# Kernel tuning notes

Hardware: AMD Instinct MI355X
Metric: run time of the kernel (lower is better)

The kernel has to match this reference:

```python
import jax, jax.numpy as jnp
import numpy as np

D_MODEL = 1024
NUM_HEADS = 16
D_K = D_MODEL // NUM_HEADS
S, B = 2048, 2


def setup_inputs() -> dict:
    key = jax.random.key(0)
    ks = jax.random.split(key, 11)
    lim = 1.0 / np.sqrt(D_MODEL)
    def lin(kw, kb):
        W = jax.random.uniform(kw, (D_MODEL, D_MODEL), jnp.float32, -lim, lim)
        b = jax.random.uniform(kb, (D_MODEL,), jnp.float32, -lim, lim)
        return W, b
    Wq, bq = lin(ks[0], ks[1])
    Wk, bk = lin(ks[2], ks[3])
    Wv, bv = lin(ks[4], ks[5])
    Wo, bo = lin(ks[6], ks[7])
    q = jax.random.normal(ks[8], (S, B, D_MODEL), jnp.float32)
    k = jax.random.normal(ks[9], (S, B, D_MODEL), jnp.float32)
    v = jax.random.normal(ks[10], (S, B, D_MODEL), jnp.float32)
    return {"q": q, "k": k, "v": v,
            "Wq": Wq, "bq": bq, "Wk": Wk, "bk": bk,
            "Wv": Wv, "bv": bv, "Wo": Wo, "bo": bo}


def reference(q, k, v, Wq, bq, Wk, bk, Wv, bv, Wo, bo):
    s, b, _ = q.shape
    scale = np.sqrt(D_K).astype(np.float32)
    # torch Linear: x @ W.T + b
    def proj(x, W, bias):
        y = jnp.einsum('sbd,ed->sbe', x, W) + bias
        # [S,B,D] -> [B,H,S,d_k]
        return y.reshape(s, b, NUM_HEADS, D_K).transpose(1, 2, 0, 3)
    Q = proj(q, Wq, bq)
    K = proj(k, Wk, bk)
    V = proj(v, Wv, bv)
    scores = jnp.einsum('bhsd,bhtd->bhst', Q, K) / scale  # [B,H,S,S]
    attn = jax.nn.softmax(scores, axis=-1)
    ctx = jnp.einsum('bhst,bhtd->bhsd', attn, V)  # [B,H,S,d_k]
    ctx = ctx.transpose(2, 0, 1, 3).reshape(s, b, NUM_HEADS * D_K)
    return jnp.einsum('sbd,ed->sbe', ctx, Wo) + bo
```

## Files before the change

kernel.cpp:

```cpp
#include <hip/hip_runtime.h>
#include <stdint.h>

typedef __attribute__((ext_vector_type(8))) short short8;
typedef __attribute__((ext_vector_type(4))) float f32x4;
typedef __attribute__((ext_vector_type(16))) float f32x16;

#define MFMA16(a, b, c) __builtin_amdgcn_mfma_f32_16x16x32_bf16((a), (b), (c), 0, 0, 0)
#define MFMA32(a, b, c) __builtin_amdgcn_mfma_f32_32x32x16_bf16((a), (b), (c), 0, 0, 0)

__device__ inline unsigned short f2bf(float x) {
  unsigned u = __float_as_uint(x);
  u = (u + 0x7FFFu + ((u >> 16) & 1u)) >> 16;
  return (unsigned short)u;
}

__device__ inline void gload16(const unsigned short* g, unsigned short* l) {
  __builtin_amdgcn_global_load_lds(
      (const __attribute__((address_space(1))) unsigned int*)g,
      (__attribute__((address_space(3))) unsigned int*)l, 16, 0, 0);
}

__device__ inline short8 lds8(const unsigned short* base, int byteoff) {
  return *reinterpret_cast<const short8*>(reinterpret_cast<const char*>(base) + byteoff);
}

__device__ inline unsigned cvtpk(float lo, float hi) {
  unsigned r;
  asm("v_cvt_pk_bf16_f32 %0, %1, %2" : "=v"(r) : "v"(lo), "v"(hi));
  return r;
}
__device__ inline void plswap(unsigned& a, unsigned& b) {
  asm volatile("v_permlane32_swap_b32 %0, %1" : "+v"(a), "+v"(b));
}
__device__ inline float swapadd(float v) {
  float a = v, b;
  asm volatile("v_mov_b32 %1, %0\n\tv_permlane32_swap_b32 %0, %1" : "+v"(a), "=&v"(b));
  return a + b;
}

__device__ inline short8 mk8(unsigned a, unsigned b, unsigned c, unsigned d) {
  union { unsigned u[4]; short8 v; } x;
  x.u[0] = a; x.u[1] = b; x.u[2] = c; x.u[3] = d;
  return x.v;
}

__device__ inline int swz(int row, int chunk) {
  return row * 128 + (((chunk) ^ (row & 7)) << 4);
}

__device__ inline void exppack(const f32x16& sv, float& lsum, short8& paLo, short8& paHi) {
  float p[16];
#pragma unroll
  for (int i = 0; i < 16; ++i) p[i] = __builtin_amdgcn_exp2f(sv[i]);
  float q8[8];
#pragma unroll
  for (int i = 0; i < 8; ++i) q8[i] = p[2 * i] + p[2 * i + 1];
#pragma unroll
  for (int s2 = 4; s2 > 0; s2 >>= 1)
#pragma unroll
    for (int i = 0; i < s2; ++i) q8[i] += q8[i + s2];
  lsum += q8[0];
  unsigned w0 = cvtpk(p[0], p[1]), w1 = cvtpk(p[2], p[3]);
  unsigned w2 = cvtpk(p[4], p[5]), w3 = cvtpk(p[6], p[7]);
  plswap(w0, w2); plswap(w1, w3);
  unsigned w4 = cvtpk(p[8], p[9]), w5 = cvtpk(p[10], p[11]);
  unsigned w6 = cvtpk(p[12], p[13]), w7 = cvtpk(p[14], p[15]);
  plswap(w4, w6); plswap(w5, w7);
  paLo = mk8(w0, w1, w2, w3);
  paHi = mk8(w4, w5, w6, w7);
}

__global__ __launch_bounds__(256) void cvt_bf16x(const float* __restrict__ a0,
                                                 const float* __restrict__ a1,
                                                 const float* __restrict__ a2,
                                                 const float* __restrict__ a3,
                                                 unsigned short* __restrict__ d, int per) {
  int y = blockIdx.y;
  const float* s = (y == 0) ? a0 : (y == 1) ? a1 : (y == 2) ? a2 : a3;
  int i = (blockIdx.x * 256 + threadIdx.x) * 8;
  if (i >= per) return;
  float4 v0 = *reinterpret_cast<const float4*>(s + i);
  float4 v1 = *reinterpret_cast<const float4*>(s + i + 4);
  short8 o;
  o[0] = (short)f2bf(v0.x); o[1] = (short)f2bf(v0.y);
  o[2] = (short)f2bf(v0.z); o[3] = (short)f2bf(v0.w);
  o[4] = (short)f2bf(v1.x); o[5] = (short)f2bf(v1.y);
  o[6] = (short)f2bf(v1.z); o[7] = (short)f2bf(v1.w);
  *reinterpret_cast<short8*>(d + (size_t)y * per + i) = o;
}

template <int MODE>
__global__ __launch_bounds__(256) void gemm_bt(
    const unsigned short* __restrict__ Abase, const unsigned short* __restrict__ Wbase,
    const float* __restrict__ bias0, const float* __restrict__ bias1,
    const float* __restrict__ bias2, unsigned short* __restrict__ ObaseBf,
    float* __restrict__ ObaseF, int M, int N, int K) {
  constexpr int CHUNK = (MODE == 0) ? 192 : 64;

  const int orig = blockIdx.x;
  const int wg = (orig & 7) * CHUNK + (orig >> 3);
  int z, bx, by;
  if (MODE == 0) {
    z = wg >> 9;
    int r = wg & 511;
    by = r & 15;
    bx = r >> 4;
  } else {
    z = 0; by = wg & 15; bx = wg >> 4;
  }

  const unsigned short* A = Abase + (size_t)z * M * K;
  const unsigned short* W = Wbase + (size_t)z * N * K;
  const float* bias = (z == 0) ? bias0 : (z == 1 ? bias1 : bias2);

  __shared__ unsigned short As[2 * 128 * 64];
  __shared__ unsigned short Bs[2 * 64 * 64];

  const int t = threadIdx.x;
  const int lane = t & 63, w = t >> 6;
  const int wm = w >> 1, wn = w & 1;
  const int m0 = bx * 128, n0 = by * 64;
  const int lrow = lane & 15, lg = lane >> 4;

  f32x4 acc[4][2] = {};

  int arow[4], acol[4], brow[2], bcol[2];
#pragma unroll
  for (int p = 0; p < 4; ++p) {
    int c = (p * 4 + w) * 64 + lane;
    arow[p] = c >> 3; acol[p] = ((c & 7) ^ (arow[p] & 7)) * 8;
  }
#pragma unroll
  for (int p = 0; p < 2; ++p) {
    int c = (p * 4 + w) * 64 + lane;
    brow[p] = c >> 3; bcol[p] = ((c & 7) ^ (brow[p] & 7)) * 8;
  }

#define STAGE_G(kt, buf)                                                              \
  {                                                                                   \
    _Pragma("unroll") for (int p = 0; p < 4; ++p)                                     \
        gload16(&A[(size_t)(m0 + arow[p]) * K + (kt) + acol[p]],                      \
                &As[(buf)*8192 + ((p * 4 + w) * 64) * 8]);                            \
    _Pragma("unroll") for (int p = 0; p < 2; ++p)                                     \
        gload16(&W[(size_t)(n0 + brow[p]) * K + (kt) + bcol[p]],                      \
                &Bs[(buf)*4096 + ((p * 4 + w) * 64) * 8]);                            \
  }

#define COMPUTE(buf)                                                                  \
  {                                                                                   \
    _Pragma("unroll") for (int kc = 0; kc < 2; ++kc) {                                \
      short8 af[4], bfr[2];                                                           \
      _Pragma("unroll") for (int i = 0; i < 4; ++i)                                   \
          af[i] = lds8(As, (buf)*16384 + swz(wm * 64 + i * 16 + lrow, kc * 4 + lg));  \
      _Pragma("unroll") for (int i = 0; i < 2; ++i)                                   \
          bfr[i] = lds8(Bs, (buf)*8192 + swz(wn * 32 + i * 16 + lrow, kc * 4 + lg));  \
      _Pragma("unroll") for (int mi = 0; mi < 4; ++mi)                                \
          _Pragma("unroll") for (int ni = 0; ni < 2; ++ni)                            \
              acc[mi][ni] = MFMA16(af[mi], bfr[ni], acc[mi][ni]);                     \
    }                                                                                 \
  }

  STAGE_G(0, 0);
  asm volatile("s_waitcnt vmcnt(0)" ::: "memory");
  __builtin_amdgcn_s_barrier();
  __builtin_amdgcn_sched_barrier(0);

  int cur = 0;
  for (int kt = 0; kt < K - 64; kt += 64) {
    STAGE_G(kt + 64, cur ^ 1);
    COMPUTE(cur);
    asm volatile("s_waitcnt vmcnt(0)" ::: "memory");
    __builtin_amdgcn_s_barrier();
    __builtin_amdgcn_sched_barrier(0);
    cur ^= 1;
  }
  COMPUTE(cur);
#undef STAGE_G
#undef COMPUTE

  const int r0 = lg * 4;
  if (MODE == 0) {
    const float scale = (z == 0) ? 0.18033688011112042f : 1.0f;
    if (z < 2) {
      unsigned short* O = ObaseBf + (size_t)z * (size_t)M * N;
#pragma unroll
      for (int mi = 0; mi < 4; ++mi)
#pragma unroll
        for (int ni = 0; ni < 2; ++ni) {
          int e = n0 + wn * 32 + ni * 16 + lrow;
          float be = bias[e];
          int h = e >> 6, d = e & 63;
#pragma unroll
          for (int r = 0; r < 4; ++r) {
            int m = m0 + wm * 64 + mi * 16 + r0 + r;
            int s = m >> 1, bb = m & 1;
            O[(((size_t)(bb * 16 + h) * 2048 + s) << 6) + d] = f2bf((acc[mi][ni][r] + be) * scale);
          }
        }
    } else {
      __builtin_amdgcn_s_barrier();
      unsigned short* T = As;
      const int h = n0 >> 6;
#pragma unroll
      for (int mi = 0; mi < 4; ++mi)
#pragma unroll
        for (int ni = 0; ni < 2; ++ni) {
          int d = wn * 32 + ni * 16 + lrow;
          float be = bias[n0 + d];
#pragma unroll
          for (int r = 0; r < 4; ++r) {
            int mrel = wm * 64 + mi * 16 + r0 + r;
            int sl = mrel >> 1, bb = mrel & 1;
            T[(bb * 64 + d) * 72 + sl] = f2bf(acc[mi][ni][r] + be);
          }
        }
      __builtin_amdgcn_s_barrier();
      unsigned short* O = ObaseBf + (size_t)2 * (size_t)M * N;
#pragma unroll
      for (int pass = 0; pass < 4; ++pass) {
        int rr = pass * 32 + (t >> 3);
        int sl8 = (t & 7) * 8;
        short8 vv = *reinterpret_cast<const short8*>(&T[rr * 72 + sl8]);
        int bb = rr >> 6, d = rr & 63;
        *reinterpret_cast<short8*>(
            &O[(((size_t)(bb * 16 + h) * 64 + d) << 11) + (m0 >> 1) + sl8]) = vv;
      }
    }
  } else {
    float* O = ObaseF;
#pragma unroll
    for (int mi = 0; mi < 4; ++mi)
#pragma unroll
      for (int ni = 0; ni < 2; ++ni) {
        int e = n0 + wn * 32 + ni * 16 + lrow;
        float be = bias[e];
#pragma unroll
        for (int r = 0; r < 4; ++r) {
          int m = m0 + wm * 64 + mi * 16 + r0 + r;
          O[(size_t)m * N + e] = acc[mi][ni][r] + be;
        }
      }
  }
}

__global__ __launch_bounds__(256, 2) void attn(const unsigned short* __restrict__ Q,
                                               const unsigned short* __restrict__ K,
                                               const unsigned short* __restrict__ Vt,
                                               unsigned short* __restrict__ ctx) {
  __shared__ unsigned short Ks[2 * 8192];
  __shared__ unsigned short Vs[2 * 8192];

  const int orig = blockIdx.x;
  const int wg = ((orig & 7) << 6) + (orig >> 3);
  const int bh = wg >> 4;
  const int qb = wg & 15;

  const int t = threadIdx.x, lane = t & 63, wv = t >> 6;
  const int q0 = qb * 128 + wv * 32;
  const int q = lane & 31, hi = lane >> 5;
  const int fq = (q ^ (q >> 3)) & 7;

  const unsigned short* Qb = Q + ((size_t)bh * 2048 + q0) * 64;
  const unsigned short* Kb = K + (size_t)bh * 2048 * 64;
  const unsigned short* Vb = Vt + (size_t)bh * 64 * 2048;

  short8 qf[4];
#pragma unroll
  for (int m = 0; m < 4; ++m)
    qf[m] = *reinterpret_cast<const short8*>(&Qb[q * 64 + m * 16 + hi * 8]);

  int koff[4][4];
#pragma unroll
  for (int st = 0; st < 4; ++st) {
    int f = fq ^ ((st & 1) * 4);
#pragma unroll
    for (int m = 0; m < 4; ++m)
      koff[st][m] = (st * 32 + q) * 128 + (((m * 2 + hi) ^ f) << 4);
  }
  int voff[2][4][2];
#pragma unroll
  for (int dh = 0; dh < 2; ++dh) {
    int g = fq ^ (dh * 4);
#pragma unroll
    for (int st = 0; st < 4; ++st)
#pragma unroll
      for (int kc = 0; kc < 2; ++kc) {
        int cir = st * 4 + kc * 2 + hi;
        int scir = (cir & 8) | ((cir & 7) ^ g);
        voff[dh][st][kc] = (dh * 32 + q) * 256 + (scir << 4);
      }
  }

  const unsigned short* ksp[4];
  const unsigned short* vpp[4];
#pragma unroll
  for (int p = 0; p < 4; ++p) {
    int c = (p * 4 + wv) * 64 + lane;
    int kr = c >> 3, kcc = c & 7;
    int gk = (kr ^ (kr >> 3)) & 7;
    ksp[p] = Kb + (size_t)kr * 64 + (kcc ^ gk) * 8;
    int vr = c >> 4, cir = c & 15;
    int gv = (vr ^ (vr >> 3)) & 7;
    int scir = (cir & 8) | ((cir & 7) ^ gv);
    vpp[p] = Vb + (size_t)vr * 2048 + scir * 8;
  }

#define STAGE(buf)                                                           \
  {                                                                          \
    _Pragma("unroll") for (int p = 0; p < 4; ++p)                            \
        gload16(ksp[p], &Ks[(buf)*8192 + ((p * 4 + wv) * 64) * 8]);          \
    _Pragma("unroll") for (int p = 0; p < 4; ++p)                            \
        gload16(vpp[p], &Vs[(buf)*8192 + ((p * 4 + wv) * 64) * 8]);          \
    _Pragma("unroll") for (int p = 0; p < 4; ++p) { ksp[p] += 8192; vpp[p] += 128; } \
  }

#define QK(st, sv)                                                           \
  {                                                                          \
    _Pragma("unroll") for (int m = 0; m < 4; ++m)                            \
        sv = MFMA32(lds8(Ks, cb + koff[st][m]), qf[m], sv);                  \
  }

#define PV(st, pl, ph)                                                       \
  {                                                                          \
    oa0 = MFMA32(pl, lds8(Vs, cb + voff[0][st][0]), oa0);                    \
    oa1 = MFMA32(pl, lds8(Vs, cb + voff[1][st][0]), oa1);                    \
    oa0 = MFMA32(ph, lds8(Vs, cb + voff[0][st][1]), oa0);                    \
    oa1 = MFMA32(ph, lds8(Vs, cb + voff[1][st][1]), oa1);                    \
  }

  f32x16 oa0 = {}, oa1 = {};
  float lsum = 0.f;

  STAGE(0);
  asm volatile("s_waitcnt vmcnt(0)" ::: "memory");
  __builtin_amdgcn_s_barrier();
  __builtin_amdgcn_sched_barrier(0);

  for (int tile = 0; tile < 16; ++tile) {
    const int cb = (tile & 1) * 16384;
    if (tile < 15) STAGE((tile & 1) ^ 1);

    __builtin_amdgcn_s_setprio(1);
    f32x16 s0 = {}, s1 = {}, s2 = {}, s3 = {};
    short8 pl, ph;
    QK(0, s0);
    QK(1, s1);
    exppack(s0, lsum, pl, ph);
    PV(0, pl, ph);
    QK(2, s2);
    exppack(s1, lsum, pl, ph);
    PV(1, pl, ph);
    QK(3, s3);
    exppack(s2, lsum, pl, ph);
    PV(2, pl, ph);
    exppack(s3, lsum, pl, ph);
    PV(3, pl, ph);
    __builtin_amdgcn_s_setprio(0);

    if (tile < 15) {
      asm volatile("s_waitcnt vmcnt(0)" ::: "memory");
      __builtin_amdgcn_sched_barrier(0);
      __builtin_amdgcn_s_barrier();
      __builtin_amdgcn_sched_barrier(0);
    }
  }
#undef STAGE
#undef QK
#undef PV

  lsum = swapadd(lsum);
  float linv = 1.0f / lsum;
  const int b = bh >> 4, h = bh & 15;
#pragma unroll
  for (int r = 0; r < 16; ++r) {
    int qr = (r & 3) + 8 * (r >> 2) + 4 * hi;
    float li = __shfl(linv, qr);
    size_t base = ((size_t)(q0 + qr) * 2 + b) * 1024 + h * 64 + q;
    ctx[base] = f2bf(oa0[r] * li);
    ctx[base + 32] = f2bf(oa1[r] * li);
  }
}

extern "C" void kernel_launch(void* const* d_in, const int* in_sizes, int n_in, void* d_out,
                              int out_size, void* d_ws, size_t ws_size, hipStream_t stream) {
  const float* q  = (const float*)d_in[0];
  const float* k  = (const float*)d_in[1];
  const float* v  = (const float*)d_in[2];
  const float* Wq = (const float*)d_in[3];
  const float* bq = (const float*)d_in[4];
  const float* Wk = (const float*)d_in[5];
  const float* bk = (const float*)d_in[6];
  const float* Wv = (const float*)d_in[7];
  const float* bv = (const float*)d_in[8];
  const float* Wo = (const float*)d_in[9];
  const float* bo = (const float*)d_in[10];

  const size_t SZ_IN = 4194304;
  const size_t SZ_W  = 1048576;
  unsigned short* ws  = (unsigned short*)d_ws;
  unsigned short* xb  = ws;
  unsigned short* Wb  = xb + 3 * SZ_IN;
  unsigned short* QKV = Wb + 4 * SZ_W;
  unsigned short* ctx = QKV + 3 * SZ_IN;

  cvt_bf16x<<<dim3(SZ_IN / 2048, 3), 256, 0, stream>>>(q, k, v, v, xb, (int)SZ_IN);
  cvt_bf16x<<<dim3(SZ_W / 2048, 4), 256, 0, stream>>>(Wq, Wk, Wv, Wo, Wb, (int)SZ_W);

  gemm_bt<0><<<1536, 256, 0, stream>>>(xb, Wb, bq, bk, bv, QKV, nullptr, 4096, 1024, 1024);
  attn<<<512, 256, 0, stream>>>(QKV, QKV + SZ_IN, QKV + 2 * SZ_IN, ctx);
  gemm_bt<1><<<512, 256, 0, stream>>>(ctx, Wb + 3 * SZ_W, bo, bo, bo, nullptr,
                                      (float*)d_out, 4096, 1024, 1024);
}
```

Baseline: 116.1 us.

## Split attention key range across wave pairs and double the grid

The attention kernel now covers 64 queries per block instead of 128, so it launches twice as many blocks. Within each block, two waves share a query group and each handles half of every 64-key tile. Their partial outputs and row sums are combined through LDS at the end. LDS use per block is halved and the launch bound is raised, aiming for higher occupancy and better spread across CUs. In exchange, each block stages K/V for fewer queries, which doubles total K/V traffic, and the final reduction adds extra synchronisation.

```diff
diff --git a/kernel.cpp b/kernel.cpp
--- a/kernel.cpp
+++ b/kernel.cpp
@@ -243,20 +243,21 @@
   }
 }
 
-__global__ __launch_bounds__(256, 2) void attn(const unsigned short* __restrict__ Q,
+__global__ __launch_bounds__(256, 5) void attn(const unsigned short* __restrict__ Q,
                                                const unsigned short* __restrict__ K,
                                                const unsigned short* __restrict__ Vt,
                                                unsigned short* __restrict__ ctx) {
-  __shared__ unsigned short Ks[2 * 8192];
-  __shared__ unsigned short Vs[2 * 8192];
+  __shared__ unsigned short Ks[2 * 4096];
+  __shared__ unsigned short Vs[2 * 4096];
 
   const int orig = blockIdx.x;
-  const int wg = ((orig & 7) << 6) + (orig >> 3);
-  const int bh = wg >> 4;
-  const int qb = wg & 15;
+  const int wg = ((orig & 7) << 7) + (orig >> 3);
+  const int bh = wg >> 5;
+  const int qb = wg & 31;
 
   const int t = threadIdx.x, lane = t & 63, wv = t >> 6;
-  const int q0 = qb * 128 + wv * 32;
+  const int qg = wv >> 1, kside = wv & 1;
+  const int q0 = qb * 64 + qg * 32;
   const int q = lane & 31, hi = lane >> 5;
   const int fq = (q ^ (q >> 3)) & 7;
 
@@ -269,63 +270,39 @@
   for (int m = 0; m < 4; ++m)
     qf[m] = *reinterpret_cast<const short8*>(&Qb[q * 64 + m * 16 + hi * 8]);
 
-  int koff[4][4];
-#pragma unroll
-  for (int st = 0; st < 4; ++st) {
-    int f = fq ^ ((st & 1) * 4);
+  int koff[4], voff[2][2];
+  {
+    int f = fq ^ (kside * 4);
 #pragma unroll
     for (int m = 0; m < 4; ++m)
-      koff[st][m] = (st * 32 + q) * 128 + (((m * 2 + hi) ^ f) << 4);
-  }
-  int voff[2][4][2];
+      koff[m] = (kside * 32 + q) * 128 + (((m * 2 + hi) ^ f) << 4);
+  }
 #pragma unroll
   for (int dh = 0; dh < 2; ++dh) {
-    int g = fq ^ (dh * 4);
-#pragma unroll
-    for (int st = 0; st < 4; ++st)
-#pragma unroll
-      for (int kc = 0; kc < 2; ++kc) {
-        int cir = st * 4 + kc * 2 + hi;
-        int scir = (cir & 8) | ((cir & 7) ^ g);
-        voff[dh][st][kc] = (dh * 32 + q) * 256 + (scir << 4);
-      }
-  }
-
-  const unsigned short* ksp[4];
-  const unsigned short* vpp[4];
-#pragma unroll
-  for (int p = 0; p < 4; ++p) {
-    int c = (p * 4 + wv) * 64 + lane;
-    int kr = c >> 3, kcc = c & 7;
-    int gk = (kr ^ (kr >> 3)) & 7;
-    ksp[p] = Kb + (size_t)kr * 64 + (kcc ^ gk) * 8;
-    int vr = c >> 4, cir = c & 15;
-    int gv = (vr ^ (vr >> 3)) & 7;
-    int scir = (cir & 8) | ((cir & 7) ^ gv);
-    vpp[p] = Vb + (size_t)vr * 2048 + scir * 8;
-  }
-
-#define STAGE(buf)                                                           \
-  {                                                                          \
-    _Pragma("unroll") for (int p = 0; p < 4; ++p)                            \
-        gload16(ksp[p], &Ks[(buf)*8192 + ((p * 4 + wv) * 64) * 8]);          \
-    _Pragma("unroll") for (int p = 0; p < 4; ++p)                            \
-        gload16(vpp[p], &Vs[(buf)*8192 + ((p * 4 + wv) * 64) * 8]);          \
-    _Pragma("unroll") for (int p = 0; p < 4; ++p) { ksp[p] += 8192; vpp[p] += 128; } \
-  }
-
-#define QK(st, sv)                                                           \
-  {                                                                          \
-    _Pragma("unroll") for (int m = 0; m < 4; ++m)                            \
-        sv = MFMA32(lds8(Ks, cb + koff[st][m]), qf[m], sv);                  \
-  }
-
-#define PV(st, pl, ph)                                                       \
-  {                                                                          \
-    oa0 = MFMA32(pl, lds8(Vs, cb + voff[0][st][0]), oa0);                    \
-    oa1 = MFMA32(pl, lds8(Vs, cb + voff[1][st][0]), oa1);                    \
-    oa0 = MFMA32(ph, lds8(Vs, cb + voff[0][st][1]), oa0);                    \
-    oa1 = MFMA32(ph, lds8(Vs, cb + voff[1][st][1]), oa1);                    \
+    int f = fq ^ (dh * 4);
+#pragma unroll
+    for (int kc = 0; kc < 2; ++kc)
+      voff[dh][kc] = (dh * 32 + q) * 128 + (((kside * 4 + kc * 2 + hi) ^ f) << 4);
+  }
+
+  int c0 = wv * 64 + lane, c1 = (4 + wv) * 64 + lane;
+  int sr0 = c0 >> 3, sr1 = c1 >> 3;
+  int sc0c = ((c0 & 7) ^ ((sr0 ^ (sr0 >> 3)) & 7)) * 8;
+  int sc1c = ((c1 & 7) ^ ((sr1 ^ (sr1 >> 3)) & 7)) * 8;
+  const unsigned short* ks0 = Kb + (size_t)sr0 * 64 + sc0c;
+  const unsigned short* ks1 = Kb + (size_t)sr1 * 64 + sc1c;
+  const unsigned short* vp0 = Vb + (size_t)sr0 * 2048 + sc0c;
+  const unsigned short* vp1 = Vb + (size_t)sr1 * 2048 + sc1c;
+
+#define STAGE(tt)                                                      \
+  {                                                                    \
+    char* kb = (char*)Ks + ((tt) & 1) * 8192;                          \
+    char* vb2 = (char*)Vs + ((tt) & 1) * 8192;                         \
+    gload16(ks0, (unsigned short*)(kb + wv * 1024));                   \
+    gload16(ks1, (unsigned short*)(kb + (4 + wv) * 1024));             \
+    gload16(vp0, (unsigned short*)(vb2 + wv * 1024));                  \
+    gload16(vp1, (unsigned short*)(vb2 + (4 + wv) * 1024));            \
+    ks0 += 4096; ks1 += 4096; vp0 += 64; vp1 += 64;                    \
   }
 
   f32x16 oa0 = {}, oa1 = {};
@@ -336,28 +313,25 @@
   __builtin_amdgcn_s_barrier();
   __builtin_amdgcn_sched_barrier(0);
 
-  for (int tile = 0; tile < 16; ++tile) {
-    const int cb = (tile & 1) * 16384;
-    if (tile < 15) STAGE((tile & 1) ^ 1);
+  for (int tile = 0; tile < 32; ++tile) {
+    const int cb = (tile & 1) * 8192;
+    if (tile < 31) STAGE(tile + 1);
 
     __builtin_amdgcn_s_setprio(1);
-    f32x16 s0 = {}, s1 = {}, s2 = {}, s3 = {};
+    f32x16 s0 = {};
+#pragma unroll
+    for (int m = 0; m < 4; ++m) s0 = MFMA32(lds8(Ks, cb + koff[m]), qf[m], s0);
+
     short8 pl, ph;
-    QK(0, s0);
-    QK(1, s1);
     exppack(s0, lsum, pl, ph);
-    PV(0, pl, ph);
-    QK(2, s2);
-    exppack(s1, lsum, pl, ph);
-    PV(1, pl, ph);
-    QK(3, s3);
-    exppack(s2, lsum, pl, ph);
-    PV(2, pl, ph);
-    exppack(s3, lsum, pl, ph);
-    PV(3, pl, ph);
+
+    oa0 = MFMA32(pl, lds8(Vs, cb + voff[0][0]), oa0);
+    oa1 = MFMA32(pl, lds8(Vs, cb + voff[1][0]), oa1);
+    oa0 = MFMA32(ph, lds8(Vs, cb + voff[0][1]), oa0);
+    oa1 = MFMA32(ph, lds8(Vs, cb + voff[1][1]), oa1);
     __builtin_amdgcn_s_setprio(0);
 
-    if (tile < 15) {
+    if (tile < 31) {
       asm volatile("s_waitcnt vmcnt(0)" ::: "memory");
       __builtin_amdgcn_sched_barrier(0);
       __builtin_amdgcn_s_barrier();
@@ -365,19 +339,40 @@
     }
   }
 #undef STAGE
-#undef QK
-#undef PV
 
   lsum = swapadd(lsum);
-  float linv = 1.0f / lsum;
-  const int b = bh >> 4, h = bh & 15;
-#pragma unroll
-  for (int r = 0; r < 16; ++r) {
-    int qr = (r & 3) + 8 * (r >> 2) + 4 * hi;
-    float li = __shfl(linv, qr);
-    size_t base = ((size_t)(q0 + qr) * 2 + b) * 1024 + h * 64 + q;
-    ctx[base] = f2bf(oa0[r] * li);
-    ctx[base + 32] = f2bf(oa1[r] * li);
+
+  __syncthreads();
+  float* combuf = (float*)Ks;
+  float* lsb = (float*)Vs;
+  if (kside == 1) {
+#pragma unroll
+    for (int r = 0; r < 16; ++r) {
+      int qr = (r & 3) + 8 * (r >> 2) + 4 * hi;
+      combuf[(qg * 32 + qr) * 64 + q] = oa0[r];
+      combuf[(qg * 32 + qr) * 64 + 32 + q] = oa1[r];
+    }
+    if (lane < 32) lsb[qg * 32 + lane] = lsum;
+  }
+  __syncthreads();
+  if (kside == 0) {
+#pragma unroll
+    for (int r = 0; r < 16; ++r) {
+      int qr = (r & 3) + 8 * (r >> 2) + 4 * hi;
+      oa0[r] += combuf[(qg * 32 + qr) * 64 + q];
+      oa1[r] += combuf[(qg * 32 + qr) * 64 + 32 + q];
+    }
+    lsum += lsb[qg * 32 + q];
+    float linv = 1.0f / lsum;
+    const int b = bh >> 4, h = bh & 15;
+#pragma unroll
+    for (int r = 0; r < 16; ++r) {
+      int qr = (r & 3) + 8 * (r >> 2) + 4 * hi;
+      float li = __shfl(linv, qr);
+      size_t base = ((size_t)(q0 + qr) * 2 + b) * 1024 + h * 64 + q;
+      ctx[base] = f2bf(oa0[r] * li);
+      ctx[base + 32] = f2bf(oa1[r] * li);
+    }
   }
 }
 
@@ -407,7 +402,7 @@
   cvt_bf16x<<<dim3(SZ_W / 2048, 4), 256, 0, stream>>>(Wq, Wk, Wv, Wo, Wb, (int)SZ_W);
 
   gemm_bt<0><<<1536, 256, 0, stream>>>(xb, Wb, bq, bk, bv, QKV, nullptr, 4096, 1024, 1024);
-  attn<<<512, 256, 0, stream>>>(QKV, QKV + SZ_IN, QKV + 2 * SZ_IN, ctx);
+  attn<<<1024, 256, 0, stream>>>(QKV, QKV + SZ_IN, QKV + 2 * SZ_IN, ctx);
   gemm_bt<1><<<512, 256, 0, stream>>>(ctx, Wb + 3 * SZ_W, bo, bo, bo, nullptr,
                                       (float*)d_out, 4096, 1024, 1024);
 }
```

Result: slower. 123.9 us (+6.7%).
